# Kernel optimization log

Hardware: AMD Instinct MI355X
Metric: run time of the kernel (lower is better)

Reference implementation:

```python
import jax, jax.numpy as jnp
import numpy as np

N_PL = 16      # PiecewiseLin resolution
OBJECTS = 10   # top-k objects kept / max count


def plin(w, x):
    """PiecewiseLin forward: w is [N_PL+1], x is any-shape tensor in [0,1]."""
    w = jnp.abs(w)
    w = w / w.sum()
    csum = jnp.cumsum(w)                     # [N_PL+1]
    y = N_PL * x
    idx = y.astype(jnp.int32)                # trunc toward zero (x >= 0)
    f = y - jnp.trunc(y)                     # fractional part
    lo = csum[jnp.minimum(idx, N_PL)]
    hi = w[jnp.minimum(idx + 1, N_PL)]
    return lo + f * hi


def _area(box):  # box: [n, 4, o]
    return jnp.clip(box[:, 2] - box[:, 0], 0.0, None) * jnp.clip(box[:, 3] - box[:, 1], 0.0, None)


def _iou(a, b):  # a, b: [n, 4, o] -> [n, o, o]
    mn = jnp.maximum(a[:, :2, :, None], b[:, :2, None, :])
    mx = jnp.minimum(a[:, 2:, :, None], b[:, 2:, None, :])
    wh = jnp.clip(mx - mn, 0.0, None)
    inter = wh[:, 0] * wh[:, 1]
    aa = _area(a)[:, :, None]
    ab = _area(b)[:, None, :]
    return inter / (aa + ab - inter + 1e-12)


def counter_forward(boxes, attention, ws):
    n = boxes.shape[0]
    # filter_most_important: top-k by attention
    att, idx = jax.lax.top_k(attention, OBJECTS)                       # [n, o]
    idx_b = jnp.broadcast_to(idx[:, None, :], (n, 4, OBJECTS))
    boxes = jnp.take_along_axis(boxes, idx_b, axis=2)                  # [n, 4, o]
    att = jax.nn.sigmoid(att)                                          # already_sigmoided=False

    relev = att[:, :, None] * att[:, None, :]                          # [n, o, o]
    dist = 1.0 - _iou(boxes, boxes)                                    # [n, o, o]

    score = plin(ws[0], relev) * plin(ws[1], dist)
    dedup = plin(ws[3], relev) * plin(ws[4], dist)

    # deduplicate
    att_diff = jnp.abs(att[:, :, None] - att[:, None, :])              # [n, o, o]
    score_diff = jnp.abs(dedup[..., :, None] - dedup[..., None, :])    # [n, o, o, o]
    sim = plin(ws[2], 1.0 - score_diff).prod(axis=1) * plin(ws[2], 1.0 - att_diff)  # [n, o, o]
    row_sims = sim.sum(axis=2)                                         # [n, o]
    all_sims = row_sims[:, :, None] * row_sims[:, None, :]             # [n, o, o]

    score = score / all_sims
    correction = plin(ws[0], att * att) / row_sims                     # [n, o]
    total = score.sum(axis=(1, 2))[:, None] + correction.sum(axis=1, keepdims=True)  # [n, 1]
    total = jnp.sqrt(total + 1e-20)

    # to_one_hot
    s = jnp.clip(total, 0.0, float(OBJECTS))                           # [n, 1]
    i = s.astype(jnp.int32)[:, 0]
    f = s - jnp.trunc(s)
    tl = jax.nn.one_hot(jnp.minimum(i, OBJECTS), OBJECTS + 1, dtype=s.dtype)
    tr = jax.nn.one_hot(jnp.minimum(i + 1, OBJECTS), OBJECTS + 1, dtype=s.dtype)
    one_hot = (1.0 - f) * tl + f * tr                                  # [n, o+1]

    # confidence
    att_conf = jnp.abs(plin(ws[5], att) - 0.5)                         # [n, o]
    dist_conf = jnp.abs(plin(ws[6], dist) - 0.5)                       # [n, o, o]
    conf = plin(ws[7], att_conf.mean(axis=1, keepdims=True)
                + dist_conf.mean(axis=2).mean(axis=1, keepdims=True))  # [n, 1]
    return one_hot * conf                                              # [n, o+1]


def setup_inputs() -> dict:
    key = jax.random.key(0)
    k1, k2, k3 = jax.random.split(key, 3)
    n, m = 32768, 36
    boxes = jax.random.uniform(k1, (n, 4, m), dtype=jnp.float32)
    attention = jax.random.normal(k2, (n, m), dtype=jnp.float32)
    ws = jax.random.uniform(k3, (8, N_PL + 1), dtype=jnp.float32, minval=0.1, maxval=1.0)
    return {"boxes": boxes, "attention": attention, "ws": ws}


def reference(boxes, attention, ws):
    return counter_forward(boxes, attention, ws)
```

## Files before the change

kernel.cpp:

```cpp
#include <hip/hip_runtime.h>
#include <math.h>

#define N_PL 16
#define NT   17
#define OBJ  10
#define M    36
#define SPB  8
#define BLK  128
#define CSTR 12

__constant__ unsigned char c_p55[55] = {
 0x00,0x01,0x02,0x03,0x04,0x05,0x06,0x07,0x08,0x09,
 0x11,0x12,0x13,0x14,0x15,0x16,0x17,0x18,0x19,
 0x22,0x23,0x24,0x25,0x26,0x27,0x28,0x29,
 0x33,0x34,0x35,0x36,0x37,0x38,0x39,
 0x44,0x45,0x46,0x47,0x48,0x49,
 0x55,0x56,0x57,0x58,0x59,
 0x66,0x67,0x68,0x69,
 0x77,0x78,0x79,
 0x88,0x89,
 0x99};
__constant__ unsigned char c_p45[45] = {
 0x01,0x02,0x03,0x04,0x05,0x06,0x07,0x08,0x09,
 0x12,0x13,0x14,0x15,0x16,0x17,0x18,0x19,
 0x23,0x24,0x25,0x26,0x27,0x28,0x29,
 0x34,0x35,0x36,0x37,0x38,0x39,
 0x45,0x46,0x47,0x48,0x49,
 0x56,0x57,0x58,0x59,
 0x67,0x68,0x69,
 0x78,0x79,
 0x89};

__device__ __forceinline__ float plin2(const float2* tb, float x) {
    float y = 16.0f * x;
    int idx = (int)y;
    float f = y - (float)idx;
    int i0 = idx < N_PL ? idx : N_PL;
    float2 cw = tb[i0];
    return __builtin_fmaf(f, cw.y, cw.x);
}

__device__ __forceinline__ unsigned int mku(float v) {
    unsigned int b = __float_as_uint(v);
    return b ^ (0x80000000u | (unsigned int)((int)b >> 31));
}

__global__ __launch_bounds__(BLK, 6) void counter_kernel(
    const float* __restrict__ boxes,
    const float* __restrict__ attn,
    const float* __restrict__ ws,
    float* __restrict__ out,
    int n)
{
    __shared__ float2 s_tab2[8 * NT];
    __shared__ float4 s_bx[SPB][OBJ];
    __shared__ float2 s_aa[SPB][OBJ];
    __shared__ float  s_ded[SPB][CSTR * OBJ];
    __shared__ float  s_sim[SPB][CSTR * OBJ];
    __shared__ float  s_rf[SPB][OBJ];

    const int tid = threadIdx.x;
    const int g = tid & 15;
    const int p = tid >> 4;

    if (tid < 8) {
        float w[NT]; float sum = 0.f;
        #pragma unroll
        for (int k = 0; k < NT; ++k) { w[k] = fabsf(ws[tid * NT + k]); sum += w[k]; }
        float rs = 1.f / sum;
        float wn[NT];
        #pragma unroll
        for (int k = 0; k < NT; ++k) wn[k] = w[k] * rs;
        float c = 0.f;
        #pragma unroll
        for (int k = 0; k < NT; ++k) {
            c += wn[k];
            s_tab2[tid * NT + k] = make_float2(c, wn[k < N_PL ? k + 1 : N_PL]);
        }
    }

    int s = blockIdx.x * SPB + p;
    const bool active = (s < n);
    if (!active) s = n - 1;

    const float* arow = attn + (size_t)s * M;
    float mv[3]; unsigned int mu[3];
    #pragma unroll
    for (int k = 0; k < 3; ++k) {
        int e = g + 16 * k;
        bool ok = e < M;
        float v = ok ? arow[e] : 0.f;
        mv[k] = v;
        mu[k] = ok ? mku(v) : 0u;
    }
    int rnk0 = 0, rnk1 = 0, rnk2 = 0;
    #pragma unroll
    for (int c4 = 0; c4 < 9; ++c4) {
        float4 t4 = ((const float4*)arow)[c4];
        float vv[4] = {t4.x, t4.y, t4.z, t4.w};
        #pragma unroll
        for (int q = 0; q < 4; ++q) {
            int m = 4 * c4 + q;
            unsigned int uu = mku(vv[q]);
            rnk0 += (uu > mu[0] || (uu == mu[0] && m < g)) ? 1 : 0;
            rnk1 += (uu > mu[1] || (uu == mu[1] && m < g + 16)) ? 1 : 0;
            rnk2 += (uu > mu[2] || (uu == mu[2] && m < g + 32)) ? 1 : 0;
        }
    }
    int rnk[3] = {rnk0, rnk1, rnk2};

    __syncthreads();

    const float* brow = boxes + (size_t)s * (4 * M);
    float mA = 0.f;
    #pragma unroll
    for (int k = 0; k < 3; ++k) {
        int e = g + 16 * k;
        if (e < M && rnk[k] < OBJ) {
            float a = 1.f / (1.f + __expf(-mv[k]));
            int r = rnk[k];
            mA += fabsf(plin2(s_tab2 + 5 * NT, a) - 0.5f);
            float x0 = brow[e], y0 = brow[M + e], x1 = brow[2 * M + e], y1 = brow[3 * M + e];
            s_bx[p][r] = make_float4(x0, y0, x1, y1);
            s_aa[p][r] = make_float2(a, fmaxf(x1 - x0, 0.f) * fmaxf(y1 - y0, 0.f));
        }
    }
    __syncthreads();

    float mD = 0.f;
    float sc_loc[4];
    #pragma unroll
    for (int t = 0; t < 4; ++t) {
        int q = g + 16 * t;
        bool act = (q < 55);
        int pk = c_p55[act ? q : 0];
        int i = pk >> 4, j = pk & 15;
        float4 bi = s_bx[p][i], bj = s_bx[p][j];
        float2 ai = s_aa[p][i], aj = s_aa[p][j];
        float wx = fminf(bi.z, bj.z) - fmaxf(bi.x, bj.x);
        float wy = fminf(bi.w, bj.w) - fmaxf(bi.y, bj.y);
        float inter = fmaxf(wx, 0.f) * fmaxf(wy, 0.f);
        float un = ai.y + aj.y - inter + 1e-12f;
        float d = 1.f - inter * __builtin_amdgcn_rcpf(un);
        float relev = ai.x * aj.x;
        float dd = plin2(s_tab2 + 3 * NT, relev) * plin2(s_tab2 + 4 * NT, d);
        sc_loc[t] = plin2(s_tab2 + 0 * NT, relev) * plin2(s_tab2 + 1 * NT, d);
        float dc = fabsf(plin2(s_tab2 + 6 * NT, d) - 0.5f);
        if (act) {
            s_ded[p][i * CSTR + j] = dd;
            s_ded[p][j * CSTR + i] = dd;
            mD += (i != j) ? 2.f * dc : dc;
        }
    }
    __syncthreads();

    if (g < OBJ) s_sim[p][g * CSTR + g] = 0.f;
    #pragma unroll
    for (int t = 0; t < 3; ++t) {
        int q = g + 16 * t;
        bool act = (q < 45);
        int pk = c_p45[act ? q : 0];
        int i = pk >> 4, j = pk & 15;
        float2 ai = s_aa[p][i], aj = s_aa[p][j];
        float prod = plin2(s_tab2 + 2 * NT, 1.f - fabsf(ai.x - aj.x));
        const float* ci = &s_ded[p][i * CSTR];
        const float* cj = &s_ded[p][j * CSTR];
        float4 ci0 = *(const float4*)ci;
        float4 ci1 = *(const float4*)(ci + 4);
        float2 ci2 = *(const float2*)(ci + 8);
        float4 cj0 = *(const float4*)cj;
        float4 cj1 = *(const float4*)(cj + 4);
        float2 cj2 = *(const float2*)(cj + 8);
        const float2* tb2 = s_tab2 + 2 * NT;
        prod *= plin2(tb2, 1.f - fabsf(ci0.x - cj0.x));
        prod *= plin2(tb2, 1.f - fabsf(ci0.y - cj0.y));
        prod *= plin2(tb2, 1.f - fabsf(ci0.z - cj0.z));
        prod *= plin2(tb2, 1.f - fabsf(ci0.w - cj0.w));
        prod *= plin2(tb2, 1.f - fabsf(ci1.x - cj1.x));
        prod *= plin2(tb2, 1.f - fabsf(ci1.y - cj1.y));
        prod *= plin2(tb2, 1.f - fabsf(ci1.z - cj1.z));
        prod *= plin2(tb2, 1.f - fabsf(ci1.w - cj1.w));
        prod *= plin2(tb2, 1.f - fabsf(ci2.x - cj2.x));
        prod *= plin2(tb2, 1.f - fabsf(ci2.y - cj2.y));
        if (act) {
            s_sim[p][i * CSTR + j] = prod;
            s_sim[p][j * CSTR + i] = prod;
        }
    }
    __syncthreads();

    if (g < OBJ) {
        float c16 = s_tab2[2 * NT + N_PL].x;
        float c2 = c16 * c16, c4 = c2 * c2, c8 = c4 * c4;
        float diag = c8 * c2 * c16;
        const float* rw = &s_sim[p][g * CSTR];
        float4 r0 = *(const float4*)rw;
        float4 r1 = *(const float4*)(rw + 4);
        float2 r2 = *(const float2*)(rw + 8);
        float sum = diag + r0.x + r0.y + r0.z + r0.w
                         + r1.x + r1.y + r1.z + r1.w + r2.x + r2.y;
        s_rf[p][g] = 1.f / sum;
    }
    __syncthreads();

    float tot = 0.f;
    #pragma unroll
    for (int t = 0; t < 4; ++t) {
        int q = g + 16 * t;
        bool act = (q < 55);
        int pk = c_p55[act ? q : 0];
        int i = pk >> 4, j = pk & 15;
        float term = sc_loc[t] * s_rf[p][i] * s_rf[p][j];
        if (act) tot += (i != j) ? 2.f * term : term;
    }
    if (g < OBJ) {
        float ai = s_aa[p][g].x;
        tot += plin2(s_tab2 + 0 * NT, ai * ai) * s_rf[p][g];
    }
    float carg = mA * 0.1f + mD * 0.01f;
    tot  += __shfl_xor(tot, 1);  tot  += __shfl_xor(tot, 2);
    tot  += __shfl_xor(tot, 4);  tot  += __shfl_xor(tot, 8);
    carg += __shfl_xor(carg, 1); carg += __shfl_xor(carg, 2);
    carg += __shfl_xor(carg, 4); carg += __shfl_xor(carg, 8);

    float total = sqrtf(tot + 1e-20f);
    float conf = plin2(s_tab2 + 7 * NT, carg);
    float scl = fminf(fmaxf(total, 0.f), 10.f);
    int i0 = (int)scl;
    float f = scl - (float)i0;
    int lo = i0 < OBJ ? i0 : OBJ;
    int hi = (i0 + 1) < OBJ ? (i0 + 1) : OBJ;

    if (active && g <= OBJ) {
        float vv = ((g == lo) ? (1.f - f) : 0.f) + ((g == hi) ? f : 0.f);
        out[(size_t)s * (OBJ + 1) + g] = vv * conf;
    }
}

extern "C" void kernel_launch(void* const* d_in, const int* in_sizes, int n_in,
                              void* d_out, int out_size, void* d_ws, size_t ws_size,
                              hipStream_t stream) {
    const float* boxes = (const float*)d_in[0];
    const float* attn  = (const float*)d_in[1];
    const float* ws    = (const float*)d_in[2];
    float* out = (float*)d_out;
    int n = in_sizes[1] / M;
    int blocks = (n + SPB - 1) / SPB;
    hipLaunchKernelGGL(counter_kernel, dim3(blocks), dim3(BLK), 0, stream,
                       boxes, attn, ws, out, n);
}
```

Measured before the change: 86.07 us.

## Use 8 threads per sample instead of 16 with 64-thread blocks

Halves the threads assigned to each sample (16 to 8) and shrinks blocks to 64 threads, so each thread handles more attention elements, pairs and rows. This cuts idle lanes, since many of the 16 lanes had no work in several phases, and lowers the cost of the shuffle reductions. The price is more serial work and more registers per thread, with fewer waves to hide latency. The top-k rank loop now does 5 comparisons per element instead of 3.

```diff
diff --git a/kernel.cpp b/kernel.cpp
--- a/kernel.cpp
+++ b/kernel.cpp
@@ -6,7 +6,7 @@
 #define OBJ  10
 #define M    36
 #define SPB  8
-#define BLK  128
+#define BLK  64
 #define CSTR 12
 
 __constant__ unsigned char c_p55[55] = {
@@ -45,7 +45,7 @@
     return b ^ (0x80000000u | (unsigned int)((int)b >> 31));
 }
 
-__global__ __launch_bounds__(BLK, 6) void counter_kernel(
+__global__ __launch_bounds__(BLK, 4) void counter_kernel(
     const float* __restrict__ boxes,
     const float* __restrict__ attn,
     const float* __restrict__ ws,
@@ -60,8 +60,8 @@
     __shared__ float  s_rf[SPB][OBJ];
 
     const int tid = threadIdx.x;
-    const int g = tid & 15;
-    const int p = tid >> 4;
+    const int g = tid & 7;
+    const int p = tid >> 3;
 
     if (tid < 8) {
         float w[NT]; float sum = 0.f;
@@ -84,16 +84,16 @@
     if (!active) s = n - 1;
 
     const float* arow = attn + (size_t)s * M;
-    float mv[3]; unsigned int mu[3];
-    #pragma unroll
-    for (int k = 0; k < 3; ++k) {
-        int e = g + 16 * k;
+    float mv[5]; unsigned int mu[5];
+    #pragma unroll
+    for (int k = 0; k < 5; ++k) {
+        int e = g + 8 * k;
         bool ok = e < M;
         float v = ok ? arow[e] : 0.f;
         mv[k] = v;
         mu[k] = ok ? mku(v) : 0u;
     }
-    int rnk0 = 0, rnk1 = 0, rnk2 = 0;
+    int rnk[5] = {0,0,0,0,0};
     #pragma unroll
     for (int c4 = 0; c4 < 9; ++c4) {
         float4 t4 = ((const float4*)arow)[c4];
@@ -102,20 +102,19 @@
         for (int q = 0; q < 4; ++q) {
             int m = 4 * c4 + q;
             unsigned int uu = mku(vv[q]);
-            rnk0 += (uu > mu[0] || (uu == mu[0] && m < g)) ? 1 : 0;
-            rnk1 += (uu > mu[1] || (uu == mu[1] && m < g + 16)) ? 1 : 0;
-            rnk2 += (uu > mu[2] || (uu == mu[2] && m < g + 32)) ? 1 : 0;
-        }
-    }
-    int rnk[3] = {rnk0, rnk1, rnk2};
+            #pragma unroll
+            for (int k = 0; k < 5; ++k)
+                rnk[k] += (uu > mu[k] || (uu == mu[k] && m < g + 8 * k)) ? 1 : 0;
+        }
+    }
 
     __syncthreads();
 
     const float* brow = boxes + (size_t)s * (4 * M);
     float mA = 0.f;
     #pragma unroll
-    for (int k = 0; k < 3; ++k) {
-        int e = g + 16 * k;
+    for (int k = 0; k < 5; ++k) {
+        int e = g + 8 * k;
         if (e < M && rnk[k] < OBJ) {
             float a = 1.f / (1.f + __expf(-mv[k]));
             int r = rnk[k];
@@ -128,10 +127,10 @@
     __syncthreads();
 
     float mD = 0.f;
-    float sc_loc[4];
-    #pragma unroll
-    for (int t = 0; t < 4; ++t) {
-        int q = g + 16 * t;
+    float sc_loc[7];
+    #pragma unroll
+    for (int t = 0; t < 7; ++t) {
+        int q = g + 8 * t;
         bool act = (q < 55);
         int pk = c_p55[act ? q : 0];
         int i = pk >> 4, j = pk & 15;
@@ -154,10 +153,11 @@
     }
     __syncthreads();
 
-    if (g < OBJ) s_sim[p][g * CSTR + g] = 0.f;
-    #pragma unroll
-    for (int t = 0; t < 3; ++t) {
-        int q = g + 16 * t;
+    s_sim[p][g * CSTR + g] = 0.f;
+    if (g < 2) s_sim[p][(g + 8) * CSTR + (g + 8)] = 0.f;
+    #pragma unroll
+    for (int t = 0; t < 6; ++t) {
+        int q = g + 8 * t;
         bool act = (q < 45);
         int pk = c_p45[act ? q : 0];
         int i = pk >> 4, j = pk & 15;
@@ -189,39 +189,47 @@
     }
     __syncthreads();
 
-    if (g < OBJ) {
+    {
         float c16 = s_tab2[2 * NT + N_PL].x;
         float c2 = c16 * c16, c4 = c2 * c2, c8 = c4 * c4;
         float diag = c8 * c2 * c16;
-        const float* rw = &s_sim[p][g * CSTR];
-        float4 r0 = *(const float4*)rw;
-        float4 r1 = *(const float4*)(rw + 4);
-        float2 r2 = *(const float2*)(rw + 8);
-        float sum = diag + r0.x + r0.y + r0.z + r0.w
-                         + r1.x + r1.y + r1.z + r1.w + r2.x + r2.y;
-        s_rf[p][g] = 1.f / sum;
+        #pragma unroll
+        for (int rep = 0; rep < 2; ++rep) {
+            int r = g + 8 * rep;
+            if (r < OBJ) {
+                const float* rw = &s_sim[p][r * CSTR];
+                float4 r0 = *(const float4*)rw;
+                float4 r1 = *(const float4*)(rw + 4);
+                float2 r2 = *(const float2*)(rw + 8);
+                float sum = diag + r0.x + r0.y + r0.z + r0.w
+                                 + r1.x + r1.y + r1.z + r1.w + r2.x + r2.y;
+                s_rf[p][r] = 1.f / sum;
+            }
+        }
     }
     __syncthreads();
 
     float tot = 0.f;
     #pragma unroll
-    for (int t = 0; t < 4; ++t) {
-        int q = g + 16 * t;
+    for (int t = 0; t < 7; ++t) {
+        int q = g + 8 * t;
         bool act = (q < 55);
         int pk = c_p55[act ? q : 0];
         int i = pk >> 4, j = pk & 15;
         float term = sc_loc[t] * s_rf[p][i] * s_rf[p][j];
         if (act) tot += (i != j) ? 2.f * term : term;
     }
-    if (g < OBJ) {
-        float ai = s_aa[p][g].x;
-        tot += plin2(s_tab2 + 0 * NT, ai * ai) * s_rf[p][g];
+    #pragma unroll
+    for (int rep = 0; rep < 2; ++rep) {
+        int r = g + 8 * rep;
+        if (r < OBJ) {
+            float ai = s_aa[p][r].x;
+            tot += plin2(s_tab2 + 0 * NT, ai * ai) * s_rf[p][r];
+        }
     }
     float carg = mA * 0.1f + mD * 0.01f;
-    tot  += __shfl_xor(tot, 1);  tot  += __shfl_xor(tot, 2);
-    tot  += __shfl_xor(tot, 4);  tot  += __shfl_xor(tot, 8);
-    carg += __shfl_xor(carg, 1); carg += __shfl_xor(carg, 2);
-    carg += __shfl_xor(carg, 4); carg += __shfl_xor(carg, 8);
+    tot  += __shfl_xor(tot, 1);  tot  += __shfl_xor(tot, 2);  tot  += __shfl_xor(tot, 4);
+    carg += __shfl_xor(carg, 1); carg += __shfl_xor(carg, 2); carg += __shfl_xor(carg, 4);
 
     float total = sqrtf(tot + 1e-20f);
     float conf = plin2(s_tab2 + 7 * NT, carg);
@@ -231,9 +239,18 @@
     int lo = i0 < OBJ ? i0 : OBJ;
     int hi = (i0 + 1) < OBJ ? (i0 + 1) : OBJ;
 
-    if (active && g <= OBJ) {
-        float vv = ((g == lo) ? (1.f - f) : 0.f) + ((g == hi) ? f : 0.f);
-        out[(size_t)s * (OBJ + 1) + g] = vv * conf;
+    if (active) {
+        float* orow = out + (size_t)s * (OBJ + 1);
+        {
+            int c = g;
+            float vv = ((c == lo) ? (1.f - f) : 0.f) + ((c == hi) ? f : 0.f);
+            orow[c] = vv * conf;
+        }
+        if (g < 3) {
+            int c = g + 8;
+            float vv = ((c == lo) ? (1.f - f) : 0.f) + ((c == hi) ? f : 0.f);
+            orow[c] = vv * conf;
+        }
     }
 }
 
```

After: 87.50 us. Within noise of the previous version (+1.7%).
